# Kernel optimization log

Measured on AMD Instinct MI355X. Metric: run time of the kernel, lower is better.

Reference implementation:

```python
import jax, jax.numpy as jnp
import numpy as np


def setup_inputs() -> dict:
    key = jax.random.key(0)
    k1, k2, k3 = jax.random.split(key, 3)
    N = 1_000_000
    H, W, D = 704, 704, 64  # 64m x 64m x ~6m scene at grid_factor=10 cells/m
    # points spread across the grid extent (meters)
    extent = jnp.array([64.0, 64.0, 5.0], dtype=jnp.float32)
    pc1 = jax.random.uniform(k1, (1, N, 3), dtype=jnp.float32) * extent
    flow = jax.random.normal(k2, (1, N, 3), dtype=jnp.float32) * 0.1  # ~10cm flow
    dist_grid = jax.random.uniform(k3, (H, W, D), dtype=jnp.float32) * 2.0  # precomputed DT values (meters)
    grid_min = jnp.zeros((3,), dtype=jnp.float32)  # grid origin (xmin, ymin, zmin)
    return {"pc1": pc1, "flow": flow, "dist_grid": dist_grid,
            "grid_min": grid_min, "grid_factor": 10}


def _trilinear_lookup(dist_grid, pts, grid_min, grid_factor):
    # pts: [N,3]; dist_grid: [H,W,D]. Continuous voxel index, clipped to bounds
    H, W, D = dist_grid.shape
    s = (pts - grid_min) * grid_factor  # [N,3]
    sx = jnp.clip(s[:, 0], 0.0, H - 1)
    sy = jnp.clip(s[:, 1], 0.0, W - 1)
    sz = jnp.clip(s[:, 2], 0.0, D - 1)
    x0 = jnp.floor(sx).astype(jnp.int32); x1 = jnp.minimum(x0 + 1, H - 1)
    y0 = jnp.floor(sy).astype(jnp.int32); y1 = jnp.minimum(y0 + 1, W - 1)
    z0 = jnp.floor(sz).astype(jnp.int32); z1 = jnp.minimum(z0 + 1, D - 1)
    wx = sx - x0; wy = sy - y0; wz = sz - z0
    # 8-corner gather
    c000 = dist_grid[x0, y0, z0]; c001 = dist_grid[x0, y0, z1]
    c010 = dist_grid[x0, y1, z0]; c011 = dist_grid[x0, y1, z1]
    c100 = dist_grid[x1, y0, z0]; c101 = dist_grid[x1, y0, z1]
    c110 = dist_grid[x1, y1, z0]; c111 = dist_grid[x1, y1, z1]
    c00 = c000 * (1 - wz) + c001 * wz
    c01 = c010 * (1 - wz) + c011 * wz
    c10 = c100 * (1 - wz) + c101 * wz
    c11 = c110 * (1 - wz) + c111 * wz
    c0 = c00 * (1 - wy) + c01 * wy
    c1 = c10 * (1 - wy) + c11 * wy
    return c0 * (1 - wx) + c1 * wx  # [N]


def reference(pc1, flow, dist_grid, grid_min, grid_factor):
    pts = (pc1 + flow)[0]  # squeeze batch: [N,3]
    dist = _trilinear_lookup(dist_grid, pts, grid_min, jnp.float32(grid_factor))
    return dist.mean(), dist
```

## Files before the change

kernel.cpp:

```cpp
#include <hip/hip_runtime.h>
#include <hip/hip_bf16.h>


#define GH 704
#define GW 704
#define GD 64
#define PTS 4

__global__ __launch_bounds__(256, 4) void dt_loss_kernel(
    const float* __restrict__ pc1,
    const float* __restrict__ flow,
    const float* __restrict__ grid,
    const float* __restrict__ grid_min,
    const int* __restrict__ grid_factor,
    float* __restrict__ out,
    int N)
{
    const int T = gridDim.x * blockDim.x;
    const int i0 = blockIdx.x * blockDim.x + threadIdx.x;

    const float gf = (float)(*grid_factor);
    const float gmx = grid_min[0];
    const float gmy = grid_min[1];
    const float gmz = grid_min[2];

    float px[PTS], py[PTS], pz[PTS];
    bool  act[PTS];
    #pragma unroll
    for (int j = 0; j < PTS; ++j) {
        const int i = i0 + j * T;
        act[j] = (i < N);
        const int ii = act[j] ? i : 0;
        px[j] = pc1[3 * ii + 0] + flow[3 * ii + 0];
        py[j] = pc1[3 * ii + 1] + flow[3 * ii + 1];
        pz[j] = pc1[3 * ii + 2] + flow[3 * ii + 2];
    }

    float wx[PTS], wy[PTS], wz[PTS];
    float c000[PTS], c001[PTS], c010[PTS], c011[PTS];
    float c100[PTS], c101[PTS], c110[PTS], c111[PTS];
    #pragma unroll
    for (int j = 0; j < PTS; ++j) {
        float sx = (px[j] - gmx) * gf;
        float sy = (py[j] - gmy) * gf;
        float sz = (pz[j] - gmz) * gf;
        sx = fminf(fmaxf(sx, 0.0f), (float)(GH - 1));
        sy = fminf(fmaxf(sy, 0.0f), (float)(GW - 1));
        sz = fminf(fmaxf(sz, 0.0f), (float)(GD - 1));

        const int x0 = (int)sx;
        const int y0 = (int)sy;
        const int z0 = (int)sz;
        const int x1 = min(x0 + 1, GH - 1);
        const int y1 = min(y0 + 1, GW - 1);
        const int z1 = min(z0 + 1, GD - 1);

        wx[j] = sx - (float)x0;
        wy[j] = sy - (float)y0;
        wz[j] = sz - (float)z0;

        const float* p00 = grid + ((size_t)x0 * GW + (size_t)y0) * GD;
        const float* p01 = grid + ((size_t)x0 * GW + (size_t)y1) * GD;
        const float* p10 = grid + ((size_t)x1 * GW + (size_t)y0) * GD;
        const float* p11 = grid + ((size_t)x1 * GW + (size_t)y1) * GD;

        c000[j] = p00[z0]; c001[j] = p00[z1];
        c010[j] = p01[z0]; c011[j] = p01[z1];
        c100[j] = p10[z0]; c101[j] = p10[z1];
        c110[j] = p11[z0]; c111[j] = p11[z1];
    }

    float acc = 0.0f;
    #pragma unroll
    for (int j = 0; j < PTS; ++j) {
        const float c00 = c000[j] * (1.0f - wz[j]) + c001[j] * wz[j];
        const float c01 = c010[j] * (1.0f - wz[j]) + c011[j] * wz[j];
        const float c10 = c100[j] * (1.0f - wz[j]) + c101[j] * wz[j];
        const float c11 = c110[j] * (1.0f - wz[j]) + c111[j] * wz[j];
        const float c0 = c00 * (1.0f - wy[j]) + c01 * wy[j];
        const float c1 = c10 * (1.0f - wy[j]) + c11 * wy[j];
        const float v  = c0 * (1.0f - wx[j]) + c1 * wx[j];
        if (act[j]) {
            out[1 + i0 + j * T] = v;
            acc += v;
        }
    }

    float s = acc;
    #pragma unroll
    for (int off = 32; off > 0; off >>= 1)
        s += __shfl_down(s, off, 64);

    __shared__ float wsum[4];
    const int lane = threadIdx.x & 63;
    const int wid  = threadIdx.x >> 6;
    if (lane == 0) wsum[wid] = s;
    __syncthreads();
    if (threadIdx.x == 0) {
        const float part = wsum[0] + wsum[1] + wsum[2] + wsum[3];
        atomicAdd(out, part * (1.0f / (float)N));
    }
}

extern "C" void kernel_launch(void* const* d_in, const int* in_sizes, int n_in,
                              void* d_out, int out_size, void* d_ws, size_t ws_size,
                              hipStream_t stream) {
    const float* pc1        = (const float*)d_in[0];
    const float* flow       = (const float*)d_in[1];
    const float* grid       = (const float*)d_in[2];
    const float* grid_min   = (const float*)d_in[3];
    const int*   grid_factor= (const int*)d_in[4];
    float* out = (float*)d_out;

    const int N = in_sizes[0] / 3;

    hipMemsetAsync(d_out, 0, sizeof(float), stream);

    const int block = 256;
    const int threads_needed = (N + PTS - 1) / PTS;
    const int grid_sz = (threads_needed + block - 1) / block;
    dt_loss_kernel<<<grid_sz, block, 0, stream>>>(
        pc1, flow, grid, grid_min, grid_factor, out, N);
}
```

Measured before the change: 246.6 us.

## Bucket-sort points by spatial tile before trilinear gather for cache locality

Replaces the single gather kernel with a four-stage pipeline: histogram points into 32x32-cell xy buckets, scan the counts, scatter clamped coordinates and original indices into bucket order, then gather from the grid in sorted order with an XCD-aware block remapping. The aim is to turn the random 8-corner reads over the 127 MB grid into spatially local accesses that hit in L2/MALL. In exchange it adds extra passes over the points, global atomics in the scatter, scattered output writes, and a 16-byte-per-point payload in the workspace. A direct fallback kernel runs when the workspace is too small.

Result: slower. 652.0 us (+164.3%).

```diff
diff --git a/kernel.cpp b/kernel.cpp
--- a/kernel.cpp
+++ b/kernel.cpp
@@ -5,65 +5,116 @@
 #define GH 704
 #define GW 704
 #define GD 64
-#define PTS 4
-
-__global__ __launch_bounds__(256, 4) void dt_loss_kernel(
-    const float* __restrict__ pc1,
-    const float* __restrict__ flow,
-    const float* __restrict__ grid,
-    const float* __restrict__ grid_min,
-    const int* __restrict__ grid_factor,
-    float* __restrict__ out,
-    int N)
-{
-    const int T = gridDim.x * blockDim.x;
-    const int i0 = blockIdx.x * blockDim.x + threadIdx.x;
-
-    const float gf = (float)(*grid_factor);
-    const float gmx = grid_min[0];
-    const float gmy = grid_min[1];
-    const float gmz = grid_min[2];
-
-    float px[PTS], py[PTS], pz[PTS];
-    bool  act[PTS];
-    #pragma unroll
-    for (int j = 0; j < PTS; ++j) {
-        const int i = i0 + j * T;
-        act[j] = (i < N);
-        const int ii = act[j] ? i : 0;
-        px[j] = pc1[3 * ii + 0] + flow[3 * ii + 0];
-        py[j] = pc1[3 * ii + 1] + flow[3 * ii + 1];
-        pz[j] = pc1[3 * ii + 2] + flow[3 * ii + 2];
-    }
-
-    float wx[PTS], wy[PTS], wz[PTS];
-    float c000[PTS], c001[PTS], c010[PTS], c011[PTS];
-    float c100[PTS], c101[PTS], c110[PTS], c111[PTS];
-    #pragma unroll
-    for (int j = 0; j < PTS; ++j) {
-        float sx = (px[j] - gmx) * gf;
-        float sy = (py[j] - gmy) * gf;
-        float sz = (pz[j] - gmz) * gf;
+
+#define BSH   5
+#define NBX   22
+#define NBUCK (NBX * NBX)
+
+__global__ __launch_bounds__(256) void k_hist(
+    const float* __restrict__ pc1, const float* __restrict__ flow,
+    const float* __restrict__ grid_min, const int* __restrict__ grid_factor,
+    unsigned* __restrict__ keys, unsigned* __restrict__ work, int N)
+{
+    __shared__ unsigned lh[NBUCK];
+    for (int t = threadIdx.x; t < NBUCK; t += blockDim.x) lh[t] = 0;
+    __syncthreads();
+
+    const int i = blockIdx.x * blockDim.x + threadIdx.x;
+    if (i < N) {
+        const float gf = (float)(*grid_factor);
+        float sx = (pc1[3 * i + 0] + flow[3 * i + 0] - grid_min[0]) * gf;
+        float sy = (pc1[3 * i + 1] + flow[3 * i + 1] - grid_min[1]) * gf;
         sx = fminf(fmaxf(sx, 0.0f), (float)(GH - 1));
         sy = fminf(fmaxf(sy, 0.0f), (float)(GW - 1));
-        sz = fminf(fmaxf(sz, 0.0f), (float)(GD - 1));
-
         const int x0 = (int)sx;
         const int y0 = (int)sy;
-        const int z0 = (int)sz;
+        const unsigned key = (unsigned)((x0 >> BSH) * NBX + (y0 >> BSH));
+        keys[i] = key;
+        atomicAdd(&lh[key], 1u);
+    }
+    __syncthreads();
+    for (int t = threadIdx.x; t < NBUCK; t += blockDim.x) {
+        const unsigned c = lh[t];
+        if (c) atomicAdd(&work[t], c);
+    }
+}
+
+__global__ __launch_bounds__(512) void k_scan(unsigned* __restrict__ work)
+{
+    __shared__ unsigned a[512], b[512];
+    const int t = threadIdx.x;
+    a[t] = (t < NBUCK) ? work[t] : 0u;
+    __syncthreads();
+    unsigned* src = a;
+    unsigned* dst = b;
+    for (int off = 1; off < 512; off <<= 1) {
+        unsigned v = src[t];
+        if (t >= off) v += src[t - off];
+        dst[t] = v;
+        __syncthreads();
+        unsigned* tmp = src; src = dst; dst = tmp;
+    }
+    if (t < NBUCK) work[t] = (t == 0) ? 0u : src[t - 1];
+}
+
+__global__ __launch_bounds__(256) void k_scatter(
+    const float* __restrict__ pc1, const float* __restrict__ flow,
+    const float* __restrict__ grid_min, const int* __restrict__ grid_factor,
+    const unsigned* __restrict__ keys, unsigned* __restrict__ work,
+    float4* __restrict__ payload, int N)
+{
+    const int i = blockIdx.x * blockDim.x + threadIdx.x;
+    if (i >= N) return;
+    const float gf = (float)(*grid_factor);
+    float sx = (pc1[3 * i + 0] + flow[3 * i + 0] - grid_min[0]) * gf;
+    float sy = (pc1[3 * i + 1] + flow[3 * i + 1] - grid_min[1]) * gf;
+    float sz = (pc1[3 * i + 2] + flow[3 * i + 2] - grid_min[2]) * gf;
+    sx = fminf(fmaxf(sx, 0.0f), (float)(GH - 1));
+    sy = fminf(fmaxf(sy, 0.0f), (float)(GW - 1));
+    sz = fminf(fmaxf(sz, 0.0f), (float)(GD - 1));
+    const unsigned pos = atomicAdd(&work[keys[i]], 1u);
+    payload[pos] = make_float4(sx, sy, sz, __uint_as_float((unsigned)i));
+}
+
+#define K4PTS 4
+__global__ __launch_bounds__(256) void k_gather(
+    const float4* __restrict__ payload, const float* __restrict__ grid,
+    float* __restrict__ out, int N, int nlb )
+{
+    const int per = nlb >> 3;
+    const int logical = (blockIdx.x & 7) * per + (blockIdx.x >> 3);
+    const int base = logical * (256 * K4PTS) + threadIdx.x;
+
+    float sx[K4PTS], sy[K4PTS], sz[K4PTS];
+    unsigned idx[K4PTS];
+    bool act[K4PTS];
+    #pragma unroll
+    for (int j = 0; j < K4PTS; ++j) {
+        const int i = base + j * 256;
+        act[j] = (i < N);
+        const float4 p = payload[act[j] ? i : 0];
+        sx[j] = p.x; sy[j] = p.y; sz[j] = p.z;
+        idx[j] = __float_as_uint(p.w);
+    }
+
+    float wx[K4PTS], wy[K4PTS], wz[K4PTS];
+    float c000[K4PTS], c001[K4PTS], c010[K4PTS], c011[K4PTS];
+    float c100[K4PTS], c101[K4PTS], c110[K4PTS], c111[K4PTS];
+    #pragma unroll
+    for (int j = 0; j < K4PTS; ++j) {
+        const int x0 = (int)sx[j];
+        const int y0 = (int)sy[j];
+        const int z0 = (int)sz[j];
         const int x1 = min(x0 + 1, GH - 1);
         const int y1 = min(y0 + 1, GW - 1);
         const int z1 = min(z0 + 1, GD - 1);
-
-        wx[j] = sx - (float)x0;
-        wy[j] = sy - (float)y0;
-        wz[j] = sz - (float)z0;
-
+        wx[j] = sx[j] - (float)x0;
+        wy[j] = sy[j] - (float)y0;
+        wz[j] = sz[j] - (float)z0;
         const float* p00 = grid + ((size_t)x0 * GW + (size_t)y0) * GD;
         const float* p01 = grid + ((size_t)x0 * GW + (size_t)y1) * GD;
         const float* p10 = grid + ((size_t)x1 * GW + (size_t)y0) * GD;
         const float* p11 = grid + ((size_t)x1 * GW + (size_t)y1) * GD;
-
         c000[j] = p00[z0]; c001[j] = p00[z1];
         c010[j] = p01[z0]; c011[j] = p01[z1];
         c100[j] = p10[z0]; c101[j] = p10[z1];
@@ -72,7 +123,7 @@
 
     float acc = 0.0f;
     #pragma unroll
-    for (int j = 0; j < PTS; ++j) {
+    for (int j = 0; j < K4PTS; ++j) {
         const float c00 = c000[j] * (1.0f - wz[j]) + c001[j] * wz[j];
         const float c01 = c010[j] * (1.0f - wz[j]) + c011[j] * wz[j];
         const float c10 = c100[j] * (1.0f - wz[j]) + c101[j] * wz[j];
@@ -81,7 +132,7 @@
         const float c1 = c10 * (1.0f - wy[j]) + c11 * wy[j];
         const float v  = c0 * (1.0f - wx[j]) + c1 * wx[j];
         if (act[j]) {
-            out[1 + i0 + j * T] = v;
+            out[1 + idx[j]] = v;
             acc += v;
         }
     }
@@ -102,23 +153,87 @@
     }
 }
 
+__global__ __launch_bounds__(256) void dt_loss_direct(
+    const float* __restrict__ pc1, const float* __restrict__ flow,
+    const float* __restrict__ grid, const float* __restrict__ grid_min,
+    const int* __restrict__ grid_factor, float* __restrict__ out, int N)
+{
+    const int i = blockIdx.x * blockDim.x + threadIdx.x;
+    float val = 0.0f;
+    if (i < N) {
+        const float gf = (float)(*grid_factor);
+        float sx = (pc1[3 * i + 0] + flow[3 * i + 0] - grid_min[0]) * gf;
+        float sy = (pc1[3 * i + 1] + flow[3 * i + 1] - grid_min[1]) * gf;
+        float sz = (pc1[3 * i + 2] + flow[3 * i + 2] - grid_min[2]) * gf;
+        sx = fminf(fmaxf(sx, 0.0f), (float)(GH - 1));
+        sy = fminf(fmaxf(sy, 0.0f), (float)(GW - 1));
+        sz = fminf(fmaxf(sz, 0.0f), (float)(GD - 1));
+        const int x0 = (int)sx, y0 = (int)sy, z0 = (int)sz;
+        const int x1 = min(x0 + 1, GH - 1);
+        const int y1 = min(y0 + 1, GW - 1);
+        const int z1 = min(z0 + 1, GD - 1);
+        const float wx = sx - x0, wy = sy - y0, wz = sz - z0;
+        const float* p00 = grid + ((size_t)x0 * GW + (size_t)y0) * GD;
+        const float* p01 = grid + ((size_t)x0 * GW + (size_t)y1) * GD;
+        const float* p10 = grid + ((size_t)x1 * GW + (size_t)y0) * GD;
+        const float* p11 = grid + ((size_t)x1 * GW + (size_t)y1) * GD;
+        const float c00 = p00[z0] * (1 - wz) + p00[z1] * wz;
+        const float c01 = p01[z0] * (1 - wz) + p01[z1] * wz;
+        const float c10 = p10[z0] * (1 - wz) + p10[z1] * wz;
+        const float c11 = p11[z0] * (1 - wz) + p11[z1] * wz;
+        const float c0 = c00 * (1 - wy) + c01 * wy;
+        const float c1 = c10 * (1 - wy) + c11 * wy;
+        val = c0 * (1 - wx) + c1 * wx;
+        out[1 + i] = val;
+    }
+    float s = val;
+    #pragma unroll
+    for (int off = 32; off > 0; off >>= 1) s += __shfl_down(s, off, 64);
+    __shared__ float wsum[4];
+    if ((threadIdx.x & 63) == 0) wsum[threadIdx.x >> 6] = s;
+    __syncthreads();
+    if (threadIdx.x == 0)
+        atomicAdd(out, (wsum[0] + wsum[1] + wsum[2] + wsum[3]) * (1.0f / (float)N));
+}
+
 extern "C" void kernel_launch(void* const* d_in, const int* in_sizes, int n_in,
                               void* d_out, int out_size, void* d_ws, size_t ws_size,
                               hipStream_t stream) {
-    const float* pc1        = (const float*)d_in[0];
-    const float* flow       = (const float*)d_in[1];
-    const float* grid       = (const float*)d_in[2];
-    const float* grid_min   = (const float*)d_in[3];
-    const int*   grid_factor= (const int*)d_in[4];
+    const float* pc1         = (const float*)d_in[0];
+    const float* flow        = (const float*)d_in[1];
+    const float* grid        = (const float*)d_in[2];
+    const float* grid_min    = (const float*)d_in[3];
+    const int*   grid_factor = (const int*)d_in[4];
     float* out = (float*)d_out;
 
     const int N = in_sizes[0] / 3;
-
     hipMemsetAsync(d_out, 0, sizeof(float), stream);
 
+    const size_t keys_off    = 4096;
+    const size_t payload_off = keys_off + (size_t)4 * N;
+    const size_t need = payload_off + (size_t)16 * N + 64;
+
+    if (ws_size < need || (payload_off % 16) != 0) {
+        const int block = 256;
+        dt_loss_direct<<<(N + block - 1) / block, block, 0, stream>>>(
+            pc1, flow, grid, grid_min, grid_factor, out, N);
+        return;
+    }
+
+    unsigned* work    = (unsigned*)d_ws;
+    unsigned* keys    = (unsigned*)((char*)d_ws + keys_off);
+    float4*   payload = (float4*)((char*)d_ws + payload_off);
+
+    hipMemsetAsync(d_ws, 0, 2048, stream);
+
     const int block = 256;
-    const int threads_needed = (N + PTS - 1) / PTS;
-    const int grid_sz = (threads_needed + block - 1) / block;
-    dt_loss_kernel<<<grid_sz, block, 0, stream>>>(
-        pc1, flow, grid, grid_min, grid_factor, out, N);
-}
+    const int nb = (N + block - 1) / block;
+
+    k_hist<<<nb, block, 0, stream>>>(pc1, flow, grid_min, grid_factor, keys, work, N);
+    k_scan<<<1, 512, 0, stream>>>(work);
+    k_scatter<<<nb, block, 0, stream>>>(pc1, flow, grid_min, grid_factor, keys, work, payload, N);
+
+    int nlb = (N + 1024 - 1) / 1024;
+    nlb = (nlb + 7) & ~7;
+    k_gather<<<nlb, block, 0, stream>>>(payload, grid, out, N, nlb);
+}
```

## Stage points in LDS with float4 loads and fetch grid z-pairs as vectors

Applied to the files above, without the earlier changes.

Each block now loads a tile of 512 points from pc1 and flow into shared memory using coalesced float4 loads, replacing the strided 3-float loads per thread. The grid gather changes from eight scalar loads per point to four 16-byte vector loads covering an aligned z window, with the z0/z1 values chosen by register selects. A scalar fallback kernel handles N not divisible by 4. The intent is fewer memory instructions and better coalescing, at the cost of LDS use, a barrier, and wider loads that may fetch unused bytes.

New measurement: 250.9 us. About the same (+1.7%).

```diff
diff --git a/kernel.cpp b/kernel.cpp
--- a/kernel.cpp
+++ b/kernel.cpp
@@ -5,45 +5,53 @@
 #define GH 704
 #define GW 704
 #define GD 64
-#define PTS 4
+#define PTS  2
+#define TILE 512
 
-__global__ __launch_bounds__(256, 4) void dt_loss_kernel(
-    const float* __restrict__ pc1,
-    const float* __restrict__ flow,
-    const float* __restrict__ grid,
-    const float* __restrict__ grid_min,
-    const int* __restrict__ grid_factor,
-    float* __restrict__ out,
-    int N)
+typedef float uf4 __attribute__((vector_size(16), aligned(8)));
+
+__device__ __forceinline__ float sel4(uf4 f, int d) {
+    const float a = (d & 2) ? f[2] : f[0];
+    const float b = (d & 2) ? f[3] : f[1];
+    return (d & 1) ? b : a;
+}
+
+__global__ __launch_bounds__(256) void dt_loss_f4(
+    const float* __restrict__ pc1, const float* __restrict__ flow,
+    const float* __restrict__ grid, const float* __restrict__ grid_min,
+    const int* __restrict__ grid_factor, float* __restrict__ out, int N)
 {
-    const int T = gridDim.x * blockDim.x;
-    const int i0 = blockIdx.x * blockDim.x + threadIdx.x;
+    __shared__ float lp[TILE * 3];
+    __shared__ float lf[TILE * 3];
 
-    const float gf = (float)(*grid_factor);
+    const int start = blockIdx.x * TILE;
+    const int cnt   = min(TILE, N - start);
+    const int n4    = (cnt * 3) >> 2;
+    const float4* p4 = (const float4*)(pc1 + 3 * (size_t)start);
+    const float4* f4 = (const float4*)(flow + 3 * (size_t)start);
+    for (int k = threadIdx.x; k < n4; k += 256) {
+        ((float4*)lp)[k] = p4[k];
+        ((float4*)lf)[k] = f4[k];
+    }
+    __syncthreads();
+
+    const float gf  = (float)(*grid_factor);
     const float gmx = grid_min[0];
     const float gmy = grid_min[1];
     const float gmz = grid_min[2];
 
-    float px[PTS], py[PTS], pz[PTS];
-    bool  act[PTS];
+    uf4 q00[PTS], q01[PTS], q10[PTS], q11[PTS];
+    float wx[PTS], wy[PTS], wz[PTS];
+    int  d0[PTS];
+    bool act[PTS];
     #pragma unroll
     for (int j = 0; j < PTS; ++j) {
-        const int i = i0 + j * T;
-        act[j] = (i < N);
-        const int ii = act[j] ? i : 0;
-        px[j] = pc1[3 * ii + 0] + flow[3 * ii + 0];
-        py[j] = pc1[3 * ii + 1] + flow[3 * ii + 1];
-        pz[j] = pc1[3 * ii + 2] + flow[3 * ii + 2];
-    }
-
-    float wx[PTS], wy[PTS], wz[PTS];
-    float c000[PTS], c001[PTS], c010[PTS], c011[PTS];
-    float c100[PTS], c101[PTS], c110[PTS], c111[PTS];
-    #pragma unroll
-    for (int j = 0; j < PTS; ++j) {
-        float sx = (px[j] - gmx) * gf;
-        float sy = (py[j] - gmy) * gf;
-        float sz = (pz[j] - gmz) * gf;
+        const int l = threadIdx.x + j * 256;
+        act[j] = (start + l) < N;
+        const int ll = act[j] ? l : 0;
+        float sx = (lp[3 * ll + 0] + lf[3 * ll + 0] - gmx) * gf;
+        float sy = (lp[3 * ll + 1] + lf[3 * ll + 1] - gmy) * gf;
+        float sz = (lp[3 * ll + 2] + lf[3 * ll + 2] - gmz) * gf;
         sx = fminf(fmaxf(sx, 0.0f), (float)(GH - 1));
         sy = fminf(fmaxf(sy, 0.0f), (float)(GW - 1));
         sz = fminf(fmaxf(sz, 0.0f), (float)(GD - 1));
@@ -53,35 +61,42 @@
         const int z0 = (int)sz;
         const int x1 = min(x0 + 1, GH - 1);
         const int y1 = min(y0 + 1, GW - 1);
-        const int z1 = min(z0 + 1, GD - 1);
-
         wx[j] = sx - (float)x0;
         wy[j] = sy - (float)y0;
         wz[j] = sz - (float)z0;
 
-        const float* p00 = grid + ((size_t)x0 * GW + (size_t)y0) * GD;
-        const float* p01 = grid + ((size_t)x0 * GW + (size_t)y1) * GD;
-        const float* p10 = grid + ((size_t)x1 * GW + (size_t)y0) * GD;
-        const float* p11 = grid + ((size_t)x1 * GW + (size_t)y1) * GD;
+        const int zb = min(z0 & ~1, GD - 4);
+        d0[j] = z0 - zb;
 
-        c000[j] = p00[z0]; c001[j] = p00[z1];
-        c010[j] = p01[z0]; c011[j] = p01[z1];
-        c100[j] = p10[z0]; c101[j] = p10[z1];
-        c110[j] = p11[z0]; c111[j] = p11[z1];
+        const float* r00 = grid + (((x0 * GW) + y0) << 6) + zb;
+        const float* r01 = grid + (((x0 * GW) + y1) << 6) + zb;
+        const float* r10 = grid + (((x1 * GW) + y0) << 6) + zb;
+        const float* r11 = grid + (((x1 * GW) + y1) << 6) + zb;
+        q00[j] = *(const uf4*)r00;
+        q01[j] = *(const uf4*)r01;
+        q10[j] = *(const uf4*)r10;
+        q11[j] = *(const uf4*)r11;
     }
 
     float acc = 0.0f;
     #pragma unroll
     for (int j = 0; j < PTS; ++j) {
-        const float c00 = c000[j] * (1.0f - wz[j]) + c001[j] * wz[j];
-        const float c01 = c010[j] * (1.0f - wz[j]) + c011[j] * wz[j];
-        const float c10 = c100[j] * (1.0f - wz[j]) + c101[j] * wz[j];
-        const float c11 = c110[j] * (1.0f - wz[j]) + c111[j] * wz[j];
-        const float c0 = c00 * (1.0f - wy[j]) + c01 * wy[j];
-        const float c1 = c10 * (1.0f - wy[j]) + c11 * wy[j];
-        const float v  = c0 * (1.0f - wx[j]) + c1 * wx[j];
+        const int dz0 = d0[j];
+        const int dz1 = min(dz0 + 1, 3);
+        const float c000 = sel4(q00[j], dz0), c001 = sel4(q00[j], dz1);
+        const float c010 = sel4(q01[j], dz0), c011 = sel4(q01[j], dz1);
+        const float c100 = sel4(q10[j], dz0), c101 = sel4(q10[j], dz1);
+        const float c110 = sel4(q11[j], dz0), c111 = sel4(q11[j], dz1);
+
+        const float c00 = c000 * (1.0f - wz[j]) + c001 * wz[j];
+        const float c01 = c010 * (1.0f - wz[j]) + c011 * wz[j];
+        const float c10 = c100 * (1.0f - wz[j]) + c101 * wz[j];
+        const float c11 = c110 * (1.0f - wz[j]) + c111 * wz[j];
+        const float c0  = c00 * (1.0f - wy[j]) + c01 * wy[j];
+        const float c1  = c10 * (1.0f - wy[j]) + c11 * wy[j];
+        const float v   = c0 * (1.0f - wx[j]) + c1 * wx[j];
         if (act[j]) {
-            out[1 + i0 + j * T] = v;
+            out[1 + start + threadIdx.x + j * 256] = v;
             acc += v;
         }
     }
@@ -102,23 +117,69 @@
     }
 }
 
+__global__ __launch_bounds__(256) void dt_loss_direct(
+    const float* __restrict__ pc1, const float* __restrict__ flow,
+    const float* __restrict__ grid, const float* __restrict__ grid_min,
+    const int* __restrict__ grid_factor, float* __restrict__ out, int N)
+{
+    const int i = blockIdx.x * blockDim.x + threadIdx.x;
+    float val = 0.0f;
+    if (i < N) {
+        const float gf = (float)(*grid_factor);
+        float sx = (pc1[3 * i + 0] + flow[3 * i + 0] - grid_min[0]) * gf;
+        float sy = (pc1[3 * i + 1] + flow[3 * i + 1] - grid_min[1]) * gf;
+        float sz = (pc1[3 * i + 2] + flow[3 * i + 2] - grid_min[2]) * gf;
+        sx = fminf(fmaxf(sx, 0.0f), (float)(GH - 1));
+        sy = fminf(fmaxf(sy, 0.0f), (float)(GW - 1));
+        sz = fminf(fmaxf(sz, 0.0f), (float)(GD - 1));
+        const int x0 = (int)sx, y0 = (int)sy, z0 = (int)sz;
+        const int x1 = min(x0 + 1, GH - 1);
+        const int y1 = min(y0 + 1, GW - 1);
+        const int z1 = min(z0 + 1, GD - 1);
+        const float wx = sx - x0, wy = sy - y0, wz = sz - z0;
+        const float* p00 = grid + ((size_t)x0 * GW + (size_t)y0) * GD;
+        const float* p01 = grid + ((size_t)x0 * GW + (size_t)y1) * GD;
+        const float* p10 = grid + ((size_t)x1 * GW + (size_t)y0) * GD;
+        const float* p11 = grid + ((size_t)x1 * GW + (size_t)y1) * GD;
+        const float c00 = p00[z0] * (1 - wz) + p00[z1] * wz;
+        const float c01 = p01[z0] * (1 - wz) + p01[z1] * wz;
+        const float c10 = p10[z0] * (1 - wz) + p10[z1] * wz;
+        const float c11 = p11[z0] * (1 - wz) + p11[z1] * wz;
+        const float c0 = c00 * (1 - wy) + c01 * wy;
+        const float c1 = c10 * (1 - wy) + c11 * wy;
+        val = c0 * (1 - wx) + c1 * wx;
+        out[1 + i] = val;
+    }
+    float s = val;
+    #pragma unroll
+    for (int off = 32; off > 0; off >>= 1) s += __shfl_down(s, off, 64);
+    __shared__ float wsum[4];
+    if ((threadIdx.x & 63) == 0) wsum[threadIdx.x >> 6] = s;
+    __syncthreads();
+    if (threadIdx.x == 0)
+        atomicAdd(out, (wsum[0] + wsum[1] + wsum[2] + wsum[3]) * (1.0f / (float)N));
+}
+
 extern "C" void kernel_launch(void* const* d_in, const int* in_sizes, int n_in,
                               void* d_out, int out_size, void* d_ws, size_t ws_size,
                               hipStream_t stream) {
-    const float* pc1        = (const float*)d_in[0];
-    const float* flow       = (const float*)d_in[1];
-    const float* grid       = (const float*)d_in[2];
-    const float* grid_min   = (const float*)d_in[3];
-    const int*   grid_factor= (const int*)d_in[4];
+    const float* pc1         = (const float*)d_in[0];
+    const float* flow        = (const float*)d_in[1];
+    const float* grid        = (const float*)d_in[2];
+    const float* grid_min    = (const float*)d_in[3];
+    const int*   grid_factor = (const int*)d_in[4];
     float* out = (float*)d_out;
 
     const int N = in_sizes[0] / 3;
-
     hipMemsetAsync(d_out, 0, sizeof(float), stream);
 
-    const int block = 256;
-    const int threads_needed = (N + PTS - 1) / PTS;
-    const int grid_sz = (threads_needed + block - 1) / block;
-    dt_loss_kernel<<<grid_sz, block, 0, stream>>>(
+    if ((N & 3) != 0) {
+        dt_loss_direct<<<(N + 255) / 256, 256, 0, stream>>>(
+            pc1, flow, grid, grid_min, grid_factor, out, N);
+        return;
+    }
+
+    const int nb = (N + TILE - 1) / TILE;
+    dt_loss_f4<<<nb, 256, 0, stream>>>(
         pc1, flow, grid, grid_min, grid_factor, out, N);
 }
```
